# Kernel optimization log

Hardware: AMD Instinct MI355X
Metric: run time of the kernel (lower is better)

The kernel has to match this reference:

```python
import jax, jax.numpy as jnp
import numpy as np

D_MODEL = 128
DEPTH = 4
LN_EPS = 1e-5


def _ssm(x, Wi, A, Wo):
    # x: [B, L, D]; Wi: [3D, D]; A: [D]; Wo: [D, D]
    z = jnp.einsum('bld,ed->ble', x, Wi)          # [B, L, 3D]
    u, i, o = jnp.split(z, 3, axis=-1)
    iu = jax.nn.sigmoid(i) * jnp.tanh(u)          # gated input, [B, L, D]
    og = jax.nn.sigmoid(o)                        # output gate
    a = jnp.minimum(jnp.exp(A), 0.999)            # decay, [D]

    def step(s, c):
        s = a * s + c
        return s, s

    s0 = jnp.zeros((x.shape[0], x.shape[2]), x.dtype)
    _, S = jax.lax.scan(step, s0, jnp.swapaxes(iu, 0, 1))  # [L, B, D]
    y = og * jnp.swapaxes(S, 0, 1)                # [B, L, D]
    return jnp.einsum('bld,ed->ble', y, Wo)


def _scan_2d(x, Wi, A, Wo):
    # x: [N, D, H, W] -> four directional 1D scans, averaged
    N, D, H, W = x.shape
    xh = jnp.transpose(x, (0, 2, 3, 1))           # [N, H, W, D]
    lr = _ssm(xh.reshape(N * H, W, D), Wi, A, Wo).reshape(N, H, W, D)
    rl = _ssm(jnp.flip(xh, 2).reshape(N * H, W, D), Wi, A, Wo).reshape(N, H, W, D)
    rl = jnp.flip(rl, 2)
    xw = jnp.transpose(x, (0, 3, 2, 1))           # [N, W, H, D]
    ud = _ssm(xw.reshape(N * W, H, D), Wi, A, Wo).reshape(N, W, H, D)
    du = _ssm(jnp.flip(xw, 2).reshape(N * W, H, D), Wi, A, Wo).reshape(N, W, H, D)
    du = jnp.flip(du, 2)
    y = (lr + rl + jnp.transpose(ud, (0, 2, 1, 3)) + jnp.transpose(du, (0, 2, 1, 3))) / 4
    return jnp.transpose(y, (0, 3, 1, 2))         # [N, D, H, W]


def setup_inputs() -> dict:
    key = jax.random.key(0)
    ks = jax.random.split(key, 8)
    D = D_MODEL
    lin = 1.0 / np.sqrt(D)
    tok = jax.random.normal(ks[0], (8, 16, D, 32, 32), jnp.float32)
    s_inp = jax.random.normal(ks[1], (DEPTH, 3 * D, D), jnp.float32) * lin
    s_A = jax.random.normal(ks[2], (DEPTH, D), jnp.float32) * -0.1
    s_out = jax.random.normal(ks[3], (DEPTH, D, D), jnp.float32) * lin
    t_inp = jax.random.normal(ks[4], (DEPTH, 3 * D, D), jnp.float32) * lin
    t_A = jax.random.normal(ks[5], (DEPTH, D), jnp.float32) * -0.1
    t_out = jax.random.normal(ks[6], (DEPTH, D, D), jnp.float32) * lin
    ln_g = jnp.ones((D,), jnp.float32)
    ln_b = jnp.zeros((D,), jnp.float32)
    return {"tok": tok, "s_inp": s_inp, "s_A": s_A, "s_out": s_out,
            "t_inp": t_inp, "t_A": t_A, "t_out": t_out,
            "ln_g": ln_g, "ln_b": ln_b}


def reference(tok, s_inp, s_A, s_out, t_inp, t_A, t_out, ln_g, ln_b):
    B, T, D, h, w = tok.shape
    x = tok
    for l in range(DEPTH):
        xs = x.reshape(B * T, D, h, w)
        xs = _scan_2d(xs, s_inp[l], s_A[l], s_out[l]).reshape(B, T, D, h, w)
        xt = jnp.transpose(xs, (0, 3, 4, 1, 2)).reshape(B * h * w, T, D)
        xt = _ssm(xt, t_inp[l], t_A[l], t_out[l]).reshape(B, h, w, T, D)
        x = x + jnp.transpose(xt, (0, 3, 4, 1, 2))
    xn = jnp.transpose(x, (0, 1, 3, 4, 2))        # [B,T,h,w,D]
    mu = jnp.mean(xn, axis=-1, keepdims=True)
    var = jnp.var(xn, axis=-1, keepdims=True)
    xn = (xn - mu) / jnp.sqrt(var + LN_EPS) * ln_g + ln_b
    return jnp.transpose(xn, (0, 1, 4, 2, 3))     # [B,T,D,h,w]
```

## Files before the change

kernel.cpp:

```cpp
#include <hip/hip_runtime.h>
#include <hip/hip_bf16.h>
#include <math.h>

#define D_MODEL 128
#define HW      1024
#define DEPTH   4
#define NIMG    128
#define B_      8
#define T_      16
#define LN_EPSF 1e-5f

typedef short  s8  __attribute__((ext_vector_type(8)));
typedef ushort us4 __attribute__((ext_vector_type(4)));
typedef ushort us2 __attribute__((ext_vector_type(2)));
typedef float  f4  __attribute__((ext_vector_type(4)));

__device__ __forceinline__ float sig_(float x) { return 1.0f / (1.0f + __expf(-x)); }
__device__ __forceinline__ float tanh_(float x) { return 2.0f * sig_(2.0f * x) - 1.0f; }
__device__ __forceinline__ ushort f2b(float f) {
    __hip_bfloat16 h = __float2bfloat16(f);
    return *reinterpret_cast<ushort*>(&h);
}
__device__ __forceinline__ float b2f(ushort u) {
    __hip_bfloat16 h = *reinterpret_cast<__hip_bfloat16*>(&u);
    return __bfloat162float(h);
}

__global__ __launch_bounds__(256) void wconv_kernel(
    const float* __restrict__ src, ushort* __restrict__ dst, int n)
{
    int i = blockIdx.x * 256 + threadIdx.x;
    if (i < n) dst[i] = f2b(src[i]);
}

__device__ __forceinline__ void gates_from_lds(
    const ushort (*Xs)[136], const ushort* __restrict__ Wi,
    ushort* __restrict__ iu, ushort* __restrict__ og,
    size_t nbase, int q0, int tid)
{
    const int lane = tid & 63;
    const int wv   = tid >> 6;
    const int grp  = lane >> 4;
    const int lrow = lane & 15;
    const int ch0  = wv * 32;

    f4 aU[4][2], aI[4][2], aO[4][2];
    #pragma unroll
    for (int mt = 0; mt < 4; ++mt)
        #pragma unroll
        for (int nt = 0; nt < 2; ++nt) { aU[mt][nt] = (f4)0.f; aI[mt][nt] = (f4)0.f; aO[mt][nt] = (f4)0.f; }

    #pragma unroll
    for (int kk = 0; kk < 4; ++kk) {
        const int kb = kk * 32 + grp * 8;
        s8 xa[4], wu[2], wi[2], wo[2];
        #pragma unroll
        for (int mt = 0; mt < 4; ++mt)
            xa[mt] = *reinterpret_cast<const s8*>(&Xs[mt * 16 + lrow][kb]);
        #pragma unroll
        for (int nt = 0; nt < 2; ++nt) {
            const int e = ch0 + nt * 16 + lrow;
            wu[nt] = *reinterpret_cast<const s8*>(Wi + (size_t)e * D_MODEL + kb);
            wi[nt] = *reinterpret_cast<const s8*>(Wi + (size_t)(e + 128) * D_MODEL + kb);
            wo[nt] = *reinterpret_cast<const s8*>(Wi + (size_t)(e + 256) * D_MODEL + kb);
        }
        #pragma unroll
        for (int mt = 0; mt < 4; ++mt)
            #pragma unroll
            for (int nt = 0; nt < 2; ++nt) {
                aU[mt][nt] = __builtin_amdgcn_mfma_f32_16x16x32_bf16(xa[mt], wu[nt], aU[mt][nt], 0, 0, 0);
                aI[mt][nt] = __builtin_amdgcn_mfma_f32_16x16x32_bf16(xa[mt], wi[nt], aI[mt][nt], 0, 0, 0);
                aO[mt][nt] = __builtin_amdgcn_mfma_f32_16x16x32_bf16(xa[mt], wo[nt], aO[mt][nt], 0, 0, 0);
            }
    }

    #pragma unroll
    for (int mt = 0; mt < 4; ++mt)
        #pragma unroll
        for (int nt = 0; nt < 2; ++nt) {
            const int e = ch0 + nt * 16 + lrow;
            const size_t off = nbase + (size_t)e * HW + q0 + mt * 16 + grp * 4;
            us4 piu, pog;
            #pragma unroll
            for (int i = 0; i < 4; ++i) {
                piu[i] = f2b(sig_(aI[mt][nt][i]) * tanh_(aU[mt][nt][i]));
                pog[i] = f2b(sig_(aO[mt][nt][i]));
            }
            *reinterpret_cast<us4*>(iu + off) = piu;
            *reinterpret_cast<us4*>(og + off) = pog;
        }
}

__global__ __launch_bounds__(256, 2) void gates_f32_kernel(
    const float* __restrict__ in, const ushort* __restrict__ Wi,
    ushort* __restrict__ iu, ushort* __restrict__ og)
{
    __shared__ ushort Xs[64][136];
    const int n   = blockIdx.x >> 4;
    const int q0  = (blockIdx.x & 15) << 6;
    const int tid = threadIdx.x;
    const size_t nbase = (size_t)n * (D_MODEL * HW);

    {
        const float* inb = in + nbase + q0;
        const int q   = tid & 63;
        const int dh0 = tid >> 6;
        for (int it = 0; it < 4; ++it) {
            const int dh = dh0 + it * 4;
            s8 pk;
            #pragma unroll
            for (int j = 0; j < 8; ++j)
                pk[j] = (short)f2b(inb[(size_t)(dh * 8 + j) * HW + q]);
            *reinterpret_cast<s8*>(&Xs[q][dh * 8]) = pk;
        }
    }
    __syncthreads();
    gates_from_lds(Xs, Wi, iu, og, nbase, q0, tid);
}

__global__ __launch_bounds__(256, 2) void fusedA_kernel(
    const ushort* __restrict__ S, const ushort* __restrict__ og_in,
    const ushort* __restrict__ Wo, const ushort* __restrict__ Wi2,
    ushort* __restrict__ iu, ushort* __restrict__ og, float scale)
{
    __shared__ ushort Gs[64][136];
    const int n   = blockIdx.x >> 4;
    const int q0  = (blockIdx.x & 15) << 6;
    const int tid = threadIdx.x;
    const size_t nbase = (size_t)n * (D_MODEL * HW);

    {
        const ushort* Sb = S     + nbase + q0;
        const ushort* Ob = og_in + nbase + q0;
        const int q   = tid & 63;
        const int dh0 = tid >> 6;
        for (int it = 0; it < 4; ++it) {
            const int dh = dh0 + it * 4;
            s8 pk;
            #pragma unroll
            for (int j = 0; j < 8; ++j) {
                const size_t o = (size_t)(dh * 8 + j) * HW + q;
                pk[j] = (short)f2b(b2f(Ob[o]) * b2f(Sb[o]) * scale);
            }
            *reinterpret_cast<s8*>(&Gs[q][dh * 8]) = pk;
        }
    }
    __syncthreads();

    const int lane = tid & 63;
    const int wv   = tid >> 6;
    const int grp  = lane >> 4;
    const int lrow = lane & 15;
    const int ch0  = wv * 32;

    f4 c1[2][4];
    #pragma unroll
    for (int et = 0; et < 2; ++et)
        #pragma unroll
        for (int qt = 0; qt < 4; ++qt) c1[et][qt] = (f4)0.f;

    #pragma unroll
    for (int kk = 0; kk < 4; ++kk) {
        const int kb = kk * 32 + grp * 8;
        s8 wf[2], xg[4];
        #pragma unroll
        for (int et = 0; et < 2; ++et)
            wf[et] = *reinterpret_cast<const s8*>(Wo + (size_t)(ch0 + et * 16 + lrow) * D_MODEL + kb);
        #pragma unroll
        for (int qt = 0; qt < 4; ++qt)
            xg[qt] = *reinterpret_cast<const s8*>(&Gs[qt * 16 + lrow][kb]);
        #pragma unroll
        for (int et = 0; et < 2; ++et)
            #pragma unroll
            for (int qt = 0; qt < 4; ++qt)
                c1[et][qt] = __builtin_amdgcn_mfma_f32_16x16x32_bf16(wf[et], xg[qt], c1[et][qt], 0, 0, 0);
    }
    __syncthreads();

    #pragma unroll
    for (int et = 0; et < 2; ++et)
        #pragma unroll
        for (int qt = 0; qt < 4; ++qt) {
            const int q = qt * 16 + lrow;
            us4 pk;
            #pragma unroll
            for (int i = 0; i < 4; ++i) pk[i] = f2b(c1[et][qt][i]);
            *reinterpret_cast<us4*>(&Gs[q][ch0 + et * 16 + grp * 4]) = pk;
        }
    __syncthreads();

    gates_from_lds(Gs, Wi2, iu, og, nbase, q0, tid);
}

template <bool GATES>
__global__ __launch_bounds__(256, 2) void fusedB_kernel(
    const ushort* __restrict__ S, const ushort* __restrict__ og_in,
    const ushort* __restrict__ Wo, const float* __restrict__ resid,
    float* __restrict__ X, const ushort* __restrict__ Wi2,
    ushort* __restrict__ iu, ushort* __restrict__ og)
{
    __shared__ ushort Gs[64][136];
    const int n   = blockIdx.x >> 4;
    const int q0  = (blockIdx.x & 15) << 6;
    const int tid = threadIdx.x;
    const size_t nbase = (size_t)n * (D_MODEL * HW);

    {
        const ushort* Sb = S     + nbase + q0;
        const ushort* Ob = og_in + nbase + q0;
        const int q   = tid & 63;
        const int dh0 = tid >> 6;
        for (int it = 0; it < 4; ++it) {
            const int dh = dh0 + it * 4;
            s8 pk;
            #pragma unroll
            for (int j = 0; j < 8; ++j) {
                const size_t o = (size_t)(dh * 8 + j) * HW + q;
                pk[j] = (short)f2b(b2f(Ob[o]) * b2f(Sb[o]));
            }
            *reinterpret_cast<s8*>(&Gs[q][dh * 8]) = pk;
        }
    }
    __syncthreads();

    const int lane = tid & 63;
    const int wv   = tid >> 6;
    const int grp  = lane >> 4;
    const int lrow = lane & 15;
    const int ch0  = wv * 32;

    f4 c1[4][2];
    #pragma unroll
    for (int mt = 0; mt < 4; ++mt)
        #pragma unroll
        for (int nt = 0; nt < 2; ++nt) c1[mt][nt] = (f4)0.f;

    #pragma unroll
    for (int kk = 0; kk < 4; ++kk) {
        const int kb = kk * 32 + grp * 8;
        s8 xg[4], wf[2];
        #pragma unroll
        for (int mt = 0; mt < 4; ++mt)
            xg[mt] = *reinterpret_cast<const s8*>(&Gs[mt * 16 + lrow][kb]);
        #pragma unroll
        for (int nt = 0; nt < 2; ++nt)
            wf[nt] = *reinterpret_cast<const s8*>(Wo + (size_t)(ch0 + nt * 16 + lrow) * D_MODEL + kb);
        #pragma unroll
        for (int mt = 0; mt < 4; ++mt)
            #pragma unroll
            for (int nt = 0; nt < 2; ++nt)
                c1[mt][nt] = __builtin_amdgcn_mfma_f32_16x16x32_bf16(xg[mt], wf[nt], c1[mt][nt], 0, 0, 0);
    }
    __syncthreads();

    #pragma unroll
    for (int mt = 0; mt < 4; ++mt)
        #pragma unroll
        for (int nt = 0; nt < 2; ++nt) {
            const int e    = ch0 + nt * 16 + lrow;
            const int qloc = mt * 16 + grp * 4;
            const size_t off = nbase + (size_t)e * HW + q0 + qloc;
            f4 r = *reinterpret_cast<const f4*>(resid + off);
            f4 v;
            #pragma unroll
            for (int i = 0; i < 4; ++i) v[i] = c1[mt][nt][i] + r[i];
            *reinterpret_cast<f4*>(X + off) = v;
            if constexpr (GATES) {
                #pragma unroll
                for (int i = 0; i < 4; ++i) Gs[qloc + i][e] = f2b(v[i]);
            }
        }

    if constexpr (GATES) {
        __syncthreads();
        gates_from_lds(Gs, Wi2, iu, og, nbase, q0, tid);
    }
}

__global__ __launch_bounds__(128) void scan2d_kernel(
    ushort* __restrict__ buf, const float* __restrict__ Avec)
{
    __shared__ float L[4][32][33];
    __shared__ float S[4][32][33];
    const int pl = threadIdx.x >> 5;
    const int r  = threadIdx.x & 31;
    const int plane = blockIdx.x * 4 + pl;
    const int d = plane & (D_MODEL - 1);
    ushort* base = buf + (size_t)plane * HW;
    const float a = fminf(__expf(Avec[d]), 0.999f);

    for (int k = 0; k < 32; ++k) L[pl][k][r] = b2f(base[k * 32 + r]);
    __syncthreads();

    {
        float acc[32];
        float s = 0.f;
        #pragma unroll
        for (int j = 0; j < 32; ++j) { s = fmaf(a, s, L[pl][r][j]); acc[j] = s; }
        s = 0.f;
        #pragma unroll
        for (int j = 31; j >= 0; --j) { s = fmaf(a, s, L[pl][r][j]); acc[j] += s; }
        #pragma unroll
        for (int j = 0; j < 32; ++j) S[pl][r][j] = acc[j];
    }
    __syncthreads();
    {
        float s = 0.f;
        #pragma unroll
        for (int i = 0; i < 32; ++i) { s = fmaf(a, s, L[pl][i][r]); S[pl][i][r] += s; }
        s = 0.f;
        #pragma unroll
        for (int i = 31; i >= 0; --i) { s = fmaf(a, s, L[pl][i][r]); S[pl][i][r] += s; }
    }
    __syncthreads();
    for (int k = 0; k < 32; ++k) base[k * 32 + r] = f2b(S[pl][k][r]);
}

__global__ __launch_bounds__(256) void tscan_kernel(
    ushort* __restrict__ buf, const float* __restrict__ Avec)
{
    const int idx = blockIdx.x * 256 + threadIdx.x;
    const int qh = idx & 511;
    const int d  = (idx >> 9) & 127;
    const int b  = idx >> 16;
    const float a = fminf(__expf(Avec[d]), 0.999f);
    size_t base = (size_t)b * (T_ * D_MODEL * HW) + (size_t)d * HW + qh * 2;
    float s0 = 0.f, s1 = 0.f;
    for (int t = 0; t < T_; ++t) {
        ushort* p = buf + base + (size_t)t * (D_MODEL * HW);
        us2 v = *reinterpret_cast<us2*>(p);
        s0 = fmaf(a, s0, b2f(v[0]));
        s1 = fmaf(a, s1, b2f(v[1]));
        us2 w; w[0] = f2b(s0); w[1] = f2b(s1);
        *reinterpret_cast<us2*>(p) = w;
    }
}

__global__ __launch_bounds__(256) void ln_kernel(
    float* __restrict__ X, const float* __restrict__ g, const float* __restrict__ b)
{
    const int p = blockIdx.x * 256 + threadIdx.x;
    if (p >= NIMG * HW) return;
    const int q = p & (HW - 1);
    const int n = p >> 10;
    const size_t base = (size_t)n * (D_MODEL * HW) + q;
    float sum = 0.f, sumsq = 0.f;
    for (int d = 0; d < D_MODEL; ++d) {
        const float x = X[base + (size_t)d * HW];
        sum += x; sumsq += x * x;
    }
    const float mean = sum * (1.f / D_MODEL);
    const float var  = sumsq * (1.f / D_MODEL) - mean * mean;
    const float rstd = rsqrtf(var + LN_EPSF);
    for (int d = 0; d < D_MODEL; ++d) {
        const size_t idx = base + (size_t)d * HW;
        X[idx] = (X[idx] - mean) * rstd * g[d] + b[d];
    }
}

extern "C" void kernel_launch(void* const* d_in, const int* in_sizes, int n_in,
                              void* d_out, int out_size, void* d_ws, size_t ws_size,
                              hipStream_t stream) {
    const float* tok   = (const float*)d_in[0];
    const float* s_inp = (const float*)d_in[1];
    const float* s_A   = (const float*)d_in[2];
    const float* s_out = (const float*)d_in[3];
    const float* t_inp = (const float*)d_in[4];
    const float* t_A   = (const float*)d_in[5];
    const float* t_out = (const float*)d_in[6];
    const float* ln_g  = (const float*)d_in[7];
    const float* ln_b  = (const float*)d_in[8];

    float*  X    = (float*)d_out;
    ushort* Abuf = (ushort*)d_ws;
    ushort* Bbuf = Abuf + (size_t)16777216;
    ushort* Wbf  = Bbuf + (size_t)16777216;
    ushort* sWiB = Wbf;
    ushort* sWoB = Wbf + 196608;
    ushort* tWiB = Wbf + 262144;
    ushort* tWoB = Wbf + 458752;

    const dim3 blk256(256), blk128(128);

    wconv_kernel<<<768, blk256, 0, stream>>>(s_inp, sWiB, 196608);
    wconv_kernel<<<256, blk256, 0, stream>>>(s_out, sWoB, 65536);
    wconv_kernel<<<768, blk256, 0, stream>>>(t_inp, tWiB, 196608);
    wconv_kernel<<<256, blk256, 0, stream>>>(t_out, tWoB, 65536);

    gates_f32_kernel<<<2048, blk256, 0, stream>>>(tok, sWiB, Abuf, Bbuf);

    for (int l = 0; l < DEPTH; ++l) {
        const float* xin = (l == 0) ? tok : X;

        scan2d_kernel<<<4096, blk128, 0, stream>>>(Abuf, s_A + (size_t)l * 128);
        fusedA_kernel<<<2048, blk256, 0, stream>>>(
            Abuf, Bbuf, sWoB + (size_t)l * 16384, tWiB + (size_t)l * 49152,
            Abuf, Bbuf, 0.25f);
        tscan_kernel<<<2048, blk256, 0, stream>>>(Abuf, t_A + (size_t)l * 128);

        if (l < DEPTH - 1) {
            fusedB_kernel<true><<<2048, blk256, 0, stream>>>(
                Abuf, Bbuf, tWoB + (size_t)l * 16384, xin, X,
                sWiB + (size_t)(l + 1) * 49152, Abuf, Bbuf);
        } else {
            fusedB_kernel<false><<<2048, blk256, 0, stream>>>(
                Abuf, Bbuf, tWoB + (size_t)l * 16384, xin, X,
                nullptr, nullptr, nullptr);
        }
    }
    ln_kernel<<<512, blk256, 0, stream>>>(X, ln_g, ln_b);
}
```

Before: 707.2 us.

## Switch intermediates to channel-last layout, split 2D scan, fuse LayerNorm into final kernel

Stores the gate and state intermediates in position-major (channel-contiguous) layout instead of channel-major. This lets the A/B kernels load gated fragments straight from global memory with 16-byte vectors, skipping the LDS transpose. The 2D scan kernel is replaced by a row-scan and a column-scan kernel that use an extra workspace buffer, and the temporal scan now uses 8-wide vector accesses. The final LayerNorm is fused into the last fusedB kernel using lane shuffles, removing a separate pass over X. The cost is an extra full-size buffer and another round of global traffic between the row and column scans.

```diff
diff --git a/kernel.cpp b/kernel.cpp
--- a/kernel.cpp
+++ b/kernel.cpp
@@ -11,8 +11,8 @@
 #define LN_EPSF 1e-5f
 
 typedef short  s8  __attribute__((ext_vector_type(8)));
+typedef ushort us8 __attribute__((ext_vector_type(8)));
 typedef ushort us4 __attribute__((ext_vector_type(4)));
-typedef ushort us2 __attribute__((ext_vector_type(2)));
 typedef float  f4  __attribute__((ext_vector_type(4)));
 
 __device__ __forceinline__ float sig_(float x) { return 1.0f / (1.0f + __expf(-x)); }
@@ -44,19 +44,19 @@
     const int lrow = lane & 15;
     const int ch0  = wv * 32;
 
-    f4 aU[4][2], aI[4][2], aO[4][2];
-    #pragma unroll
-    for (int mt = 0; mt < 4; ++mt)
-        #pragma unroll
-        for (int nt = 0; nt < 2; ++nt) { aU[mt][nt] = (f4)0.f; aI[mt][nt] = (f4)0.f; aO[mt][nt] = (f4)0.f; }
+    f4 aU[2][4], aI[2][4], aO[2][4];
+    #pragma unroll
+    for (int nt = 0; nt < 2; ++nt)
+        #pragma unroll
+        for (int qt = 0; qt < 4; ++qt) { aU[nt][qt] = (f4)0.f; aI[nt][qt] = (f4)0.f; aO[nt][qt] = (f4)0.f; }
 
     #pragma unroll
     for (int kk = 0; kk < 4; ++kk) {
         const int kb = kk * 32 + grp * 8;
-        s8 xa[4], wu[2], wi[2], wo[2];
-        #pragma unroll
-        for (int mt = 0; mt < 4; ++mt)
-            xa[mt] = *reinterpret_cast<const s8*>(&Xs[mt * 16 + lrow][kb]);
+        s8 xb[4], wu[2], wi[2], wo[2];
+        #pragma unroll
+        for (int qt = 0; qt < 4; ++qt)
+            xb[qt] = *reinterpret_cast<const s8*>(&Xs[qt * 16 + lrow][kb]);
         #pragma unroll
         for (int nt = 0; nt < 2; ++nt) {
             const int e = ch0 + nt * 16 + lrow;
@@ -65,30 +65,48 @@
             wo[nt] = *reinterpret_cast<const s8*>(Wi + (size_t)(e + 256) * D_MODEL + kb);
         }
         #pragma unroll
-        for (int mt = 0; mt < 4; ++mt)
-            #pragma unroll
-            for (int nt = 0; nt < 2; ++nt) {
-                aU[mt][nt] = __builtin_amdgcn_mfma_f32_16x16x32_bf16(xa[mt], wu[nt], aU[mt][nt], 0, 0, 0);
-                aI[mt][nt] = __builtin_amdgcn_mfma_f32_16x16x32_bf16(xa[mt], wi[nt], aI[mt][nt], 0, 0, 0);
-                aO[mt][nt] = __builtin_amdgcn_mfma_f32_16x16x32_bf16(xa[mt], wo[nt], aO[mt][nt], 0, 0, 0);
+        for (int nt = 0; nt < 2; ++nt)
+            #pragma unroll
+            for (int qt = 0; qt < 4; ++qt) {
+                aU[nt][qt] = __builtin_amdgcn_mfma_f32_16x16x32_bf16(wu[nt], xb[qt], aU[nt][qt], 0, 0, 0);
+                aI[nt][qt] = __builtin_amdgcn_mfma_f32_16x16x32_bf16(wi[nt], xb[qt], aI[nt][qt], 0, 0, 0);
+                aO[nt][qt] = __builtin_amdgcn_mfma_f32_16x16x32_bf16(wo[nt], xb[qt], aO[nt][qt], 0, 0, 0);
             }
     }
 
     #pragma unroll
-    for (int mt = 0; mt < 4; ++mt)
-        #pragma unroll
-        for (int nt = 0; nt < 2; ++nt) {
-            const int e = ch0 + nt * 16 + lrow;
-            const size_t off = nbase + (size_t)e * HW + q0 + mt * 16 + grp * 4;
+    for (int nt = 0; nt < 2; ++nt)
+        #pragma unroll
+        for (int qt = 0; qt < 4; ++qt) {
+            const int q = q0 + qt * 16 + lrow;
+            const size_t off = nbase + (size_t)q * D_MODEL + ch0 + nt * 16 + grp * 4;
             us4 piu, pog;
             #pragma unroll
             for (int i = 0; i < 4; ++i) {
-                piu[i] = f2b(sig_(aI[mt][nt][i]) * tanh_(aU[mt][nt][i]));
-                pog[i] = f2b(sig_(aO[mt][nt][i]));
+                piu[i] = f2b(sig_(aI[nt][qt][i]) * tanh_(aU[nt][qt][i]));
+                pog[i] = f2b(sig_(aO[nt][qt][i]));
             }
             *reinterpret_cast<us4*>(iu + off) = piu;
             *reinterpret_cast<us4*>(og + off) = pog;
         }
+}
+
+__device__ __forceinline__ void stage1_gfrags(
+    const ushort* __restrict__ S, const ushort* __restrict__ og,
+    float scale, size_t nbase, int q0, int wv, int grp, int lrow, s8 g[4])
+{
+    const size_t rbase = nbase + (size_t)(q0 + wv * 16 + lrow) * D_MODEL + grp * 8;
+    #pragma unroll
+    for (int kk = 0; kk < 4; ++kk) {
+        const size_t off = rbase + kk * 32;
+        us8 sv = *reinterpret_cast<const us8*>(S + off);
+        us8 ov = *reinterpret_cast<const us8*>(og + off);
+        s8 gg;
+        #pragma unroll
+        for (int j = 0; j < 8; ++j)
+            gg[j] = (short)f2b(b2f(sv[j]) * b2f(ov[j]) * scale);
+        g[kk] = gg;
+    }
 }
 
 __global__ __launch_bounds__(256, 2) void gates_f32_kernel(
@@ -123,238 +141,208 @@
     const ushort* __restrict__ Wo, const ushort* __restrict__ Wi2,
     ushort* __restrict__ iu, ushort* __restrict__ og, float scale)
 {
-    __shared__ ushort Gs[64][136];
+    __shared__ ushort Xs[64][136];
     const int n   = blockIdx.x >> 4;
     const int q0  = (blockIdx.x & 15) << 6;
     const int tid = threadIdx.x;
+    const int lane = tid & 63, wv = tid >> 6, grp = lane >> 4, lrow = lane & 15;
     const size_t nbase = (size_t)n * (D_MODEL * HW);
 
-    {
-        const ushort* Sb = S     + nbase + q0;
-        const ushort* Ob = og_in + nbase + q0;
-        const int q   = tid & 63;
-        const int dh0 = tid >> 6;
-        for (int it = 0; it < 4; ++it) {
-            const int dh = dh0 + it * 4;
-            s8 pk;
-            #pragma unroll
-            for (int j = 0; j < 8; ++j) {
-                const size_t o = (size_t)(dh * 8 + j) * HW + q;
-                pk[j] = (short)f2b(b2f(Ob[o]) * b2f(Sb[o]) * scale);
-            }
-            *reinterpret_cast<s8*>(&Gs[q][dh * 8]) = pk;
-        }
-    }
-    __syncthreads();
-
-    const int lane = tid & 63;
-    const int wv   = tid >> 6;
-    const int grp  = lane >> 4;
-    const int lrow = lane & 15;
-    const int ch0  = wv * 32;
-
-    f4 c1[2][4];
-    #pragma unroll
-    for (int et = 0; et < 2; ++et)
-        #pragma unroll
-        for (int qt = 0; qt < 4; ++qt) c1[et][qt] = (f4)0.f;
-
+    s8 g[4];
+    stage1_gfrags(S, og_in, scale, nbase, q0, wv, grp, lrow, g);
+
+    f4 C[8];
+    #pragma unroll
+    for (int et = 0; et < 8; ++et) C[et] = (f4)0.f;
     #pragma unroll
     for (int kk = 0; kk < 4; ++kk) {
         const int kb = kk * 32 + grp * 8;
-        s8 wf[2], xg[4];
-        #pragma unroll
-        for (int et = 0; et < 2; ++et)
-            wf[et] = *reinterpret_cast<const s8*>(Wo + (size_t)(ch0 + et * 16 + lrow) * D_MODEL + kb);
-        #pragma unroll
-        for (int qt = 0; qt < 4; ++qt)
-            xg[qt] = *reinterpret_cast<const s8*>(&Gs[qt * 16 + lrow][kb]);
-        #pragma unroll
-        for (int et = 0; et < 2; ++et)
-            #pragma unroll
-            for (int qt = 0; qt < 4; ++qt)
-                c1[et][qt] = __builtin_amdgcn_mfma_f32_16x16x32_bf16(wf[et], xg[qt], c1[et][qt], 0, 0, 0);
-    }
+        #pragma unroll
+        for (int et = 0; et < 8; ++et) {
+            s8 wf = *reinterpret_cast<const s8*>(Wo + (size_t)(et * 16 + lrow) * D_MODEL + kb);
+            C[et] = __builtin_amdgcn_mfma_f32_16x16x32_bf16(g[kk], wf, C[et], 0, 0, 0);
+        }
+    }
+
+    #pragma unroll
+    for (int et = 0; et < 8; ++et)
+        #pragma unroll
+        for (int i = 0; i < 4; ++i)
+            Xs[wv * 16 + grp * 4 + i][et * 16 + lrow] = f2b(C[et][i]);
     __syncthreads();
 
-    #pragma unroll
-    for (int et = 0; et < 2; ++et)
-        #pragma unroll
-        for (int qt = 0; qt < 4; ++qt) {
-            const int q = qt * 16 + lrow;
-            us4 pk;
-            #pragma unroll
-            for (int i = 0; i < 4; ++i) pk[i] = f2b(c1[et][qt][i]);
-            *reinterpret_cast<us4*>(&Gs[q][ch0 + et * 16 + grp * 4]) = pk;
-        }
-    __syncthreads();
-
-    gates_from_lds(Gs, Wi2, iu, og, nbase, q0, tid);
-}
-
-template <bool GATES>
+    gates_from_lds(Xs, Wi2, iu, og, nbase, q0, tid);
+}
+
+template <bool GATES, bool LN>
 __global__ __launch_bounds__(256, 2) void fusedB_kernel(
     const ushort* __restrict__ S, const ushort* __restrict__ og_in,
     const ushort* __restrict__ Wo, const float* __restrict__ resid,
     float* __restrict__ X, const ushort* __restrict__ Wi2,
-    ushort* __restrict__ iu, ushort* __restrict__ og)
-{
-    __shared__ ushort Gs[64][136];
+    ushort* __restrict__ iu, ushort* __restrict__ og,
+    const float* __restrict__ lng, const float* __restrict__ lnb)
+{
+    __shared__ ushort Xs[64][136];
     const int n   = blockIdx.x >> 4;
     const int q0  = (blockIdx.x & 15) << 6;
     const int tid = threadIdx.x;
+    const int lane = tid & 63, wv = tid >> 6, grp = lane >> 4, lrow = lane & 15;
     const size_t nbase = (size_t)n * (D_MODEL * HW);
 
-    {
-        const ushort* Sb = S     + nbase + q0;
-        const ushort* Ob = og_in + nbase + q0;
-        const int q   = tid & 63;
-        const int dh0 = tid >> 6;
-        for (int it = 0; it < 4; ++it) {
-            const int dh = dh0 + it * 4;
-            s8 pk;
-            #pragma unroll
-            for (int j = 0; j < 8; ++j) {
-                const size_t o = (size_t)(dh * 8 + j) * HW + q;
-                pk[j] = (short)f2b(b2f(Ob[o]) * b2f(Sb[o]));
-            }
-            *reinterpret_cast<s8*>(&Gs[q][dh * 8]) = pk;
-        }
-    }
-    __syncthreads();
-
-    const int lane = tid & 63;
-    const int wv   = tid >> 6;
-    const int grp  = lane >> 4;
-    const int lrow = lane & 15;
-    const int ch0  = wv * 32;
-
-    f4 c1[4][2];
-    #pragma unroll
-    for (int mt = 0; mt < 4; ++mt)
-        #pragma unroll
-        for (int nt = 0; nt < 2; ++nt) c1[mt][nt] = (f4)0.f;
-
+    s8 g[4];
+    stage1_gfrags(S, og_in, 1.0f, nbase, q0, wv, grp, lrow, g);
+
+    f4 C[8];
+    #pragma unroll
+    for (int et = 0; et < 8; ++et) C[et] = (f4)0.f;
     #pragma unroll
     for (int kk = 0; kk < 4; ++kk) {
         const int kb = kk * 32 + grp * 8;
-        s8 xg[4], wf[2];
-        #pragma unroll
-        for (int mt = 0; mt < 4; ++mt)
-            xg[mt] = *reinterpret_cast<const s8*>(&Gs[mt * 16 + lrow][kb]);
-        #pragma unroll
-        for (int nt = 0; nt < 2; ++nt)
-            wf[nt] = *reinterpret_cast<const s8*>(Wo + (size_t)(ch0 + nt * 16 + lrow) * D_MODEL + kb);
-        #pragma unroll
-        for (int mt = 0; mt < 4; ++mt)
-            #pragma unroll
-            for (int nt = 0; nt < 2; ++nt)
-                c1[mt][nt] = __builtin_amdgcn_mfma_f32_16x16x32_bf16(xg[mt], wf[nt], c1[mt][nt], 0, 0, 0);
-    }
-    __syncthreads();
-
-    #pragma unroll
-    for (int mt = 0; mt < 4; ++mt)
-        #pragma unroll
-        for (int nt = 0; nt < 2; ++nt) {
-            const int e    = ch0 + nt * 16 + lrow;
-            const int qloc = mt * 16 + grp * 4;
-            const size_t off = nbase + (size_t)e * HW + q0 + qloc;
+        #pragma unroll
+        for (int et = 0; et < 8; ++et) {
+            s8 wf = *reinterpret_cast<const s8*>(Wo + (size_t)(et * 16 + lrow) * D_MODEL + kb);
+            C[et] = __builtin_amdgcn_mfma_f32_16x16x32_bf16(g[kk], wf, C[et], 0, 0, 0);
+        }
+    }
+
+    const int qb = q0 + wv * 16 + grp * 4;
+
+    if constexpr (LN) {
+        float sum[4] = {0.f, 0.f, 0.f, 0.f}, sq[4] = {0.f, 0.f, 0.f, 0.f};
+        #pragma unroll
+        for (int et = 0; et < 8; ++et) {
+            const int e = et * 16 + lrow;
+            const size_t off = nbase + (size_t)e * HW + qb;
+            f4 r = *reinterpret_cast<const f4*>(resid + off);
+            #pragma unroll
+            for (int i = 0; i < 4; ++i) {
+                float v = C[et][i] + r[i];
+                C[et][i] = v;
+                sum[i] += v; sq[i] += v * v;
+            }
+        }
+        #pragma unroll
+        for (int m = 1; m <= 8; m <<= 1)
+            #pragma unroll
+            for (int i = 0; i < 4; ++i) {
+                sum[i] += __shfl_xor(sum[i], m);
+                sq[i]  += __shfl_xor(sq[i], m);
+            }
+        float mean[4], rstd[4];
+        #pragma unroll
+        for (int i = 0; i < 4; ++i) {
+            mean[i] = sum[i] * (1.f / D_MODEL);
+            float var = sq[i] * (1.f / D_MODEL) - mean[i] * mean[i];
+            rstd[i] = rsqrtf(var + LN_EPSF);
+        }
+        #pragma unroll
+        for (int et = 0; et < 8; ++et) {
+            const int e = et * 16 + lrow;
+            const float ge = lng[e], be = lnb[e];
+            const size_t off = nbase + (size_t)e * HW + qb;
+            f4 o;
+            #pragma unroll
+            for (int i = 0; i < 4; ++i)
+                o[i] = (C[et][i] - mean[i]) * rstd[i] * ge + be;
+            *reinterpret_cast<f4*>(X + off) = o;
+        }
+    } else {
+        #pragma unroll
+        for (int et = 0; et < 8; ++et) {
+            const int e = et * 16 + lrow;
+            const size_t off = nbase + (size_t)e * HW + qb;
             f4 r = *reinterpret_cast<const f4*>(resid + off);
             f4 v;
             #pragma unroll
-            for (int i = 0; i < 4; ++i) v[i] = c1[mt][nt][i] + r[i];
+            for (int i = 0; i < 4; ++i) v[i] = C[et][i] + r[i];
             *reinterpret_cast<f4*>(X + off) = v;
             if constexpr (GATES) {
                 #pragma unroll
-                for (int i = 0; i < 4; ++i) Gs[qloc + i][e] = f2b(v[i]);
+                for (int i = 0; i < 4; ++i)
+                    Xs[wv * 16 + grp * 4 + i][e] = f2b(v[i]);
             }
         }
-
-    if constexpr (GATES) {
-        __syncthreads();
-        gates_from_lds(Gs, Wi2, iu, og, nbase, q0, tid);
-    }
-}
-
-__global__ __launch_bounds__(128) void scan2d_kernel(
-    ushort* __restrict__ buf, const float* __restrict__ Avec)
-{
-    __shared__ float L[4][32][33];
-    __shared__ float S[4][32][33];
-    const int pl = threadIdx.x >> 5;
-    const int r  = threadIdx.x & 31;
-    const int plane = blockIdx.x * 4 + pl;
-    const int d = plane & (D_MODEL - 1);
-    ushort* base = buf + (size_t)plane * HW;
-    const float a = fminf(__expf(Avec[d]), 0.999f);
-
-    for (int k = 0; k < 32; ++k) L[pl][k][r] = b2f(base[k * 32 + r]);
-    __syncthreads();
-
-    {
-        float acc[32];
-        float s = 0.f;
-        #pragma unroll
-        for (int j = 0; j < 32; ++j) { s = fmaf(a, s, L[pl][r][j]); acc[j] = s; }
-        s = 0.f;
-        #pragma unroll
-        for (int j = 31; j >= 0; --j) { s = fmaf(a, s, L[pl][r][j]); acc[j] += s; }
-        #pragma unroll
-        for (int j = 0; j < 32; ++j) S[pl][r][j] = acc[j];
-    }
-    __syncthreads();
-    {
-        float s = 0.f;
-        #pragma unroll
-        for (int i = 0; i < 32; ++i) { s = fmaf(a, s, L[pl][i][r]); S[pl][i][r] += s; }
-        s = 0.f;
-        #pragma unroll
-        for (int i = 31; i >= 0; --i) { s = fmaf(a, s, L[pl][i][r]); S[pl][i][r] += s; }
-    }
-    __syncthreads();
-    for (int k = 0; k < 32; ++k) base[k * 32 + r] = f2b(S[pl][k][r]);
+        if constexpr (GATES) {
+            __syncthreads();
+            gates_from_lds(Xs, Wi2, iu, og, nbase, q0, tid);
+        }
+    }
+}
+
+__global__ __launch_bounds__(256) void rowscan_kernel(
+    const ushort* __restrict__ iu, ushort* __restrict__ R,
+    const float* __restrict__ Av)
+{
+    const int tid = blockIdx.x * 256 + threadIdx.x;
+    const int d = tid & 127;
+    const int i = (tid >> 7) & 31;
+    const int n = tid >> 12;
+    const float a = fminf(__expf(Av[d]), 0.999f);
+    const size_t base = (size_t)n * (D_MODEL * HW) + (size_t)(i * 32) * D_MODEL + d;
+
+    float x[32], acc[32];
+    #pragma unroll
+    for (int j = 0; j < 32; ++j) x[j] = b2f(iu[base + (size_t)j * D_MODEL]);
+    float s = 0.f;
+    #pragma unroll
+    for (int j = 0; j < 32; ++j) { s = fmaf(a, s, x[j]); acc[j] = s; }
+    s = 0.f;
+    #pragma unroll
+    for (int j = 31; j >= 0; --j) { s = fmaf(a, s, x[j]); acc[j] += s; }
+    #pragma unroll
+    for (int j = 0; j < 32; ++j) R[base + (size_t)j * D_MODEL] = f2b(acc[j]);
+}
+
+__global__ __launch_bounds__(256) void colscan_kernel(
+    ushort* __restrict__ buf, const ushort* __restrict__ R,
+    const float* __restrict__ Av)
+{
+    const int tid = blockIdx.x * 256 + threadIdx.x;
+    const int d = tid & 127;
+    const int j = (tid >> 7) & 31;
+    const int n = tid >> 12;
+    const float a = fminf(__expf(Av[d]), 0.999f);
+    const size_t base = (size_t)n * (D_MODEL * HW) + (size_t)j * D_MODEL + d;
+    const size_t istr = (size_t)32 * D_MODEL;
+
+    float x[32], t[32];
+    #pragma unroll
+    for (int i = 0; i < 32; ++i) x[i] = b2f(buf[base + i * istr]);
+    float s = 0.f;
+    #pragma unroll
+    for (int i = 0; i < 32; ++i) { s = fmaf(a, s, x[i]); t[i] = s; }
+    s = 0.f;
+    #pragma unroll
+    for (int i = 31; i >= 0; --i) { s = fmaf(a, s, x[i]); t[i] += s; }
+    #pragma unroll
+    for (int i = 0; i < 32; ++i)
+        buf[base + i * istr] = f2b(t[i] + b2f(R[base + i * istr]));
 }
 
 __global__ __launch_bounds__(256) void tscan_kernel(
-    ushort* __restrict__ buf, const float* __restrict__ Avec)
-{
-    const int idx = blockIdx.x * 256 + threadIdx.x;
-    const int qh = idx & 511;
-    const int d  = (idx >> 9) & 127;
-    const int b  = idx >> 16;
-    const float a = fminf(__expf(Avec[d]), 0.999f);
-    size_t base = (size_t)b * (T_ * D_MODEL * HW) + (size_t)d * HW + qh * 2;
-    float s0 = 0.f, s1 = 0.f;
+    ushort* __restrict__ buf, const float* __restrict__ Av)
+{
+    const int tid = blockIdx.x * 256 + threadIdx.x;
+    const int dc = tid & 15;
+    const int q  = (tid >> 4) & 1023;
+    const int b  = tid >> 14;
+    float aa[8], st[8];
+    #pragma unroll
+    for (int jj = 0; jj < 8; ++jj) {
+        aa[jj] = fminf(__expf(Av[dc * 8 + jj]), 0.999f);
+        st[jj] = 0.f;
+    }
+    #pragma unroll
     for (int t = 0; t < T_; ++t) {
-        ushort* p = buf + base + (size_t)t * (D_MODEL * HW);
-        us2 v = *reinterpret_cast<us2*>(p);
-        s0 = fmaf(a, s0, b2f(v[0]));
-        s1 = fmaf(a, s1, b2f(v[1]));
-        us2 w; w[0] = f2b(s0); w[1] = f2b(s1);
-        *reinterpret_cast<us2*>(p) = w;
-    }
-}
-
-__global__ __launch_bounds__(256) void ln_kernel(
-    float* __restrict__ X, const float* __restrict__ g, const float* __restrict__ b)
-{
-    const int p = blockIdx.x * 256 + threadIdx.x;
-    if (p >= NIMG * HW) return;
-    const int q = p & (HW - 1);
-    const int n = p >> 10;
-    const size_t base = (size_t)n * (D_MODEL * HW) + q;
-    float sum = 0.f, sumsq = 0.f;
-    for (int d = 0; d < D_MODEL; ++d) {
-        const float x = X[base + (size_t)d * HW];
-        sum += x; sumsq += x * x;
-    }
-    const float mean = sum * (1.f / D_MODEL);
-    const float var  = sumsq * (1.f / D_MODEL) - mean * mean;
-    const float rstd = rsqrtf(var + LN_EPSF);
-    for (int d = 0; d < D_MODEL; ++d) {
-        const size_t idx = base + (size_t)d * HW;
-        X[idx] = (X[idx] - mean) * rstd * g[d] + b[d];
+        const size_t off = ((size_t)(b * T_ + t) * HW + q) * D_MODEL + dc * 8;
+        us8 v = *reinterpret_cast<us8*>(buf + off);
+        us8 w;
+        #pragma unroll
+        for (int jj = 0; jj < 8; ++jj) {
+            st[jj] = fmaf(aa[jj], st[jj], b2f(v[jj]));
+            w[jj] = f2b(st[jj]);
+        }
+        *reinterpret_cast<us8*>(buf + off) = w;
     }
 }
 
@@ -374,13 +362,14 @@
     float*  X    = (float*)d_out;
     ushort* Abuf = (ushort*)d_ws;
     ushort* Bbuf = Abuf + (size_t)16777216;
-    ushort* Wbf  = Bbuf + (size_t)16777216;
+    ushort* Cbuf = Bbuf + (size_t)16777216;
+    ushort* Wbf  = Cbuf + (size_t)16777216;
     ushort* sWiB = Wbf;
     ushort* sWoB = Wbf + 196608;
     ushort* tWiB = Wbf + 262144;
     ushort* tWoB = Wbf + 458752;
 
-    const dim3 blk256(256), blk128(128);
+    const dim3 blk256(256);
 
     wconv_kernel<<<768, blk256, 0, stream>>>(s_inp, sWiB, 196608);
     wconv_kernel<<<256, blk256, 0, stream>>>(s_out, sWoB, 65536);
@@ -392,21 +381,21 @@
     for (int l = 0; l < DEPTH; ++l) {
         const float* xin = (l == 0) ? tok : X;
 
-        scan2d_kernel<<<4096, blk128, 0, stream>>>(Abuf, s_A + (size_t)l * 128);
+        rowscan_kernel<<<2048, blk256, 0, stream>>>(Abuf, Cbuf, s_A + (size_t)l * 128);
+        colscan_kernel<<<2048, blk256, 0, stream>>>(Abuf, Cbuf, s_A + (size_t)l * 128);
         fusedA_kernel<<<2048, blk256, 0, stream>>>(
             Abuf, Bbuf, sWoB + (size_t)l * 16384, tWiB + (size_t)l * 49152,
             Abuf, Bbuf, 0.25f);
-        tscan_kernel<<<2048, blk256, 0, stream>>>(Abuf, t_A + (size_t)l * 128);
+        tscan_kernel<<<512, blk256, 0, stream>>>(Abuf, t_A + (size_t)l * 128);
 
         if (l < DEPTH - 1) {
-            fusedB_kernel<true><<<2048, blk256, 0, stream>>>(
+            fusedB_kernel<true, false><<<2048, blk256, 0, stream>>>(
                 Abuf, Bbuf, tWoB + (size_t)l * 16384, xin, X,
-                sWiB + (size_t)(l + 1) * 49152, Abuf, Bbuf);
+                sWiB + (size_t)(l + 1) * 49152, Abuf, Bbuf, nullptr, nullptr);
         } else {
-            fusedB_kernel<false><<<2048, blk256, 0, stream>>>(
+            fusedB_kernel<false, true><<<2048, blk256, 0, stream>>>(
                 Abuf, Bbuf, tWoB + (size_t)l * 16384, xin, X,
-                nullptr, nullptr, nullptr);
-        }
-    }
-    ln_kernel<<<512, blk256, 0, stream>>>(X, ln_g, ln_b);
-}
+                nullptr, nullptr, nullptr, ln_g, ln_b);
+        }
+    }
+}
```

After: 850.8 us. +20.3%, slower.
